# Performance work log

Measured on AMD Instinct MI355X. Metric: run time of the kernel, lower is better.

## Reference

```python
import jax, jax.numpy as jnp
import numpy as np

EMBED_DIM = 1024
KEY_SIZE = 1024
VALUE_SIZE = 1024


def setup_inputs() -> dict:
    key = jax.random.key(0)
    k1, k2, k3, k4, k5 = jax.random.split(key, 5)
    B, L = 4, 4096
    s = 1.0 / np.sqrt(EMBED_DIM)
    return {
        "x": jax.random.normal(k1, (B, L, EMBED_DIM), dtype=jnp.float32),
        # torch nn.Linear weights: [out_features, in_features]
        "Wq": jax.random.normal(k2, (KEY_SIZE, EMBED_DIM), dtype=jnp.float32) * s,
        "Wk": jax.random.normal(k3, (KEY_SIZE, EMBED_DIM), dtype=jnp.float32) * s,
        "Wv": jax.random.normal(k4, (VALUE_SIZE, EMBED_DIM), dtype=jnp.float32) * s,
        "Wo": jax.random.normal(k5, (EMBED_DIM, VALUE_SIZE), dtype=jnp.float32) * s,
    }


def reference(x, Wq, Wk, Wv, Wo):
    # x: [B, L, E]
    q = jnp.einsum("ble,ke->blk", x, Wq)  # [B, L, K]
    k = jnp.einsum("ble,ke->blk", x, Wk)  # [B, L, K]
    v = jnp.einsum("ble,ve->blv", x, Wv)  # [B, L, V]
    K = k.shape[-1]
    # transposed (feature-axial) attention: att over feature dims, contracting seq L
    att = jnp.einsum("blk,blj->bkj", q, k) / jnp.sqrt(jnp.asarray(K, x.dtype))  # [B, K, K]
    att = jax.nn.softmax(att, axis=-1)
    # out[b,l,k] = sum_j att[b,k,j] * v[b,l,j]  (matmul(att, v^T) then transpose)
    out = jnp.einsum("bkj,blj->blk", att, v)  # [B, L, K]
    return jnp.einsum("blv,ev->ble", out, Wo)  # [B, L, E]
```

## Files before the change

### kernel.cpp

```cpp
#include <hip/hip_runtime.h>
#include <hip/hip_bf16.h>

typedef unsigned short u16;
typedef __bf16 bf16x8 __attribute__((ext_vector_type(8)));
typedef float f32x4 __attribute__((ext_vector_type(4)));
typedef unsigned short ushort8 __attribute__((ext_vector_type(8)));

#define AS1 __attribute__((address_space(1)))
#define AS3 __attribute__((address_space(3)))

__device__ inline u16 f2bf(float f) {
  union { float f; unsigned int u; } c; c.f = f;
  unsigned int u = c.u;
  return (u16)((u + 0x7fffu + ((u >> 16) & 1u)) >> 16);
}
__device__ inline float bf2f(u16 v) {
  union { unsigned int u; float f; } c; c.u = ((unsigned int)v) << 16;
  return c.f;
}

__global__ __launch_bounds__(256) void cvt_x_dual(const float* __restrict__ x,
                                                  u16* __restrict__ xbf,
                                                  u16* __restrict__ xT) {
  __shared__ u16 tile[64][68];
  const int t = threadIdx.x;
  const long e0 = (long)blockIdx.x * 64;
  const long l0 = (long)blockIdx.y * 64;
  const long b  = blockIdx.z;
  const int tr = t >> 4, tc = t & 15;
#pragma unroll
  for (int i = 0; i < 4; ++i) {
    const int r = tr + i * 16;
    const long gl = b * 4096 + l0 + r;
    float4 v = *reinterpret_cast<const float4*>(x + gl * 1024 + e0 + tc * 4);
    ushort4 o;
    o.x = f2bf(v.x); o.y = f2bf(v.y); o.z = f2bf(v.z); o.w = f2bf(v.w);
    *reinterpret_cast<ushort4*>(xbf + gl * 1024 + e0 + tc * 4) = o;
    *reinterpret_cast<ushort4*>(&tile[r][tc * 4]) = o;
  }
  __syncthreads();
#pragma unroll
  for (int i = 0; i < 4; ++i) {
    const int c = tr + i * 16;
    ushort4 o;
    o.x = tile[tc * 4 + 0][c]; o.y = tile[tc * 4 + 1][c];
    o.z = tile[tc * 4 + 2][c]; o.w = tile[tc * 4 + 3][c];
    *reinterpret_cast<ushort4*>(xT + b * (1024L * 4096) + (e0 + c) * 4096 + l0 + tc * 4) = o;
  }
}

__global__ __launch_bounds__(256) void cvt_w4(const float* __restrict__ a, const float* __restrict__ b,
                                              const float* __restrict__ c, const float* __restrict__ d,
                                              u16* __restrict__ oa, u16* __restrict__ ob,
                                              u16* __restrict__ oc, u16* __restrict__ od) {
  int i = blockIdx.x * 256 + threadIdx.x;
  const int which = i >> 18;
  const int j = i & 262143;
  const float* src = which == 0 ? a : which == 1 ? b : which == 2 ? c : d;
  u16* dst = which == 0 ? oa : which == 1 ? ob : which == 2 ? oc : od;
  float4 v = reinterpret_cast<const float4*>(src)[j];
  ushort4 o;
  o.x = f2bf(v.x); o.y = f2bf(v.y); o.z = f2bf(v.z); o.w = f2bf(v.w);
  reinterpret_cast<ushort4*>(dst)[j] = o;
}

__global__ __launch_bounds__(256) void transpose_bf16(
    const u16* __restrict__ src, long sLd, long sZ,
    u16* __restrict__ dst, long dLd, long dZ) {
  __shared__ u16 tile[64][68];
  const int t = threadIdx.x;
  const long r0 = (long)blockIdx.y * 64;
  const long c0 = (long)blockIdx.x * 64;
  const long z = blockIdx.z;
  const int tr = t >> 4, tc = t & 15;
#pragma unroll
  for (int i = 0; i < 4; ++i) {
    const int r = tr + i * 16;
    ushort4 v = *reinterpret_cast<const ushort4*>(src + z * sZ + (r0 + r) * sLd + c0 + tc * 4);
    *reinterpret_cast<ushort4*>(&tile[r][tc * 4]) = v;
  }
  __syncthreads();
#pragma unroll
  for (int i = 0; i < 4; ++i) {
    const int c = tr + i * 16;
    ushort4 o;
    o.x = tile[tc * 4 + 0][c]; o.y = tile[tc * 4 + 1][c];
    o.z = tile[tc * 4 + 2][c]; o.w = tile[tc * 4 + 3][c];
    *reinterpret_cast<ushort4*>(dst + z * dZ + (c0 + c) * dLd + r0 + tc * 4) = o;
  }
}

__device__ __forceinline__ void stage_half(const u16* __restrict__ g, long ld, int k0,
                                           u16* dst, int t) {
#pragma unroll
  for (int i = 0; i < 2; ++i) {
    const int c = i * 512 + t;
    const int r = c >> 3;
    const int s = c & 7;
    const int col = ((s ^ (r & 7)) << 3) + k0;
    __builtin_amdgcn_global_load_lds((const AS1 void*)(g + (long)r * ld + col),
                                     (AS3 void*)(dst + c * 8), 16, 0, 0);
  }
}

__device__ __forceinline__ bf16x8 frag_ld(const u16* s, int row, int colb) {
  return *reinterpret_cast<const bf16x8*>(
      reinterpret_cast<const char*>(s) + row * 128 + (colb ^ ((row & 7) << 4)));
}

#define BAR_PRE()       do { asm volatile("s_waitcnt vmcnt(6)" ::: "memory"); \
                             __builtin_amdgcn_s_barrier(); \
                             asm volatile("" ::: "memory"); } while (0)
#define BAR_POST()      do { asm volatile("" ::: "memory"); \
                             __builtin_amdgcn_s_barrier(); \
                             asm volatile("" ::: "memory"); } while (0)

template<bool OUT_F32>
__global__ __launch_bounds__(512, 2) void gemm_nt256(
    const u16* __restrict__ A, long lda, long sAz4, long sAz1,
    const u16* __restrict__ B, long ldb, long sBz4, long sBz1,
    void* __restrict__ Cv, long ldc, long sCz4, long sCz1,
    long cBatch, int cShift,
    int K, float scale)
{
  __shared__ u16 sm[2 * 32768] __attribute__((aligned(16)));

  const int t = threadIdx.x;
  int wg = blockIdx.x + gridDim.x * blockIdx.y;
  const int nwg = gridDim.x * gridDim.y;
  const int qq = nwg >> 3;
  wg = (wg & 7) * qq + (wg >> 3);
  const long m0 = (long)(wg % gridDim.x) * 256;
  const long n0 = (long)(wg / gridDim.x) * 256;
  const int z = blockIdx.z;
  const long azoff = (long)(z >> 2) * sAz4 + (long)(z & 3) * sAz1;
  const long bzoff = (long)(z >> 2) * sBz4 + (long)(z & 3) * sBz1;
  const u16* Ab = A + azoff + m0 * lda;
  const u16* Bb = B + bzoff + n0 * ldb;

  const int wid = t >> 6, lane = t & 63;
  const int lhi = lane >> 4, llo = lane & 15;
  const int wm = wid >> 2, wn = wid & 3;

  f32x4 acc[2][4][2][2] = {};
  const int NT = K >> 6;

  stage_half(Ab, lda, 0, sm, t);
  stage_half(Bb + 128 * ldb, ldb, 0, sm + 16384 + 8192, t);
  stage_half(Bb, ldb, 0, sm + 16384, t);
  stage_half(Ab + 128 * lda, lda, 0, sm + 8192, t);
  stage_half(Ab, lda, 64, sm + 32768, t);
  stage_half(Bb + 128 * ldb, ldb, 64, sm + 32768 + 16384 + 8192, t);
  asm volatile("s_waitcnt vmcnt(4)" ::: "memory");
  __builtin_amdgcn_s_barrier();
  asm volatile("" ::: "memory");

  for (int kt = 0; kt < NT; ++kt) {
    const int kb = kt & 1;
    u16* bc = sm + kb * 32768;
    u16* bn = sm + (kb ^ 1) * 32768;
    const u16* sAc = bc;
    const u16* sBc = bc + 16384;
    const int k1 = ((kt + 1 < NT) ? kt + 1 : 0) << 6;
    const int k2 = ((kt + 2 < NT) ? kt + 2 : kt + 2 - NT) << 6;

    bf16x8 a[4][2], bl[2][2], bh[2][2];

#pragma unroll
    for (int fr = 0; fr < 4; ++fr)
#pragma unroll
      for (int kk = 0; kk < 2; ++kk)
        a[fr][kk] = frag_ld(sAc, wm * 64 + fr * 16 + llo, (kk << 6) + (lhi << 4));
#pragma unroll
    for (int fc = 0; fc < 2; ++fc)
#pragma unroll
      for (int kk = 0; kk < 2; ++kk)
        bl[fc][kk] = frag_ld(sBc, wn * 32 + fc * 16 + llo, (kk << 6) + (lhi << 4));
    stage_half(Bb, ldb, k1, bn + 16384, t);
    BAR_PRE();
    __builtin_amdgcn_s_setprio(1);
#pragma unroll
    for (int fr = 0; fr < 4; ++fr)
#pragma unroll
      for (int fc = 0; fc < 2; ++fc)
#pragma unroll
        for (int kk = 0; kk < 2; ++kk)
          acc[0][fr][0][fc] = __builtin_amdgcn_mfma_f32_16x16x32_bf16(a[fr][kk], bl[fc][kk], acc[0][fr][0][fc], 0, 0, 0);
    __builtin_amdgcn_s_setprio(0);
    BAR_POST();

#pragma unroll
    for (int fc = 0; fc < 2; ++fc)
#pragma unroll
      for (int kk = 0; kk < 2; ++kk)
        bh[fc][kk] = frag_ld(sBc, 128 + wn * 32 + fc * 16 + llo, (kk << 6) + (lhi << 4));
    stage_half(Ab + 128 * lda, lda, k1, bn + 8192, t);
    BAR_PRE();
    __builtin_amdgcn_s_setprio(1);
#pragma unroll
    for (int fr = 0; fr < 4; ++fr)
#pragma unroll
      for (int fc = 0; fc < 2; ++fc)
#pragma unroll
        for (int kk = 0; kk < 2; ++kk)
          acc[0][fr][1][fc] = __builtin_amdgcn_mfma_f32_16x16x32_bf16(a[fr][kk], bh[fc][kk], acc[0][fr][1][fc], 0, 0, 0);
    __builtin_amdgcn_s_setprio(0);
    BAR_POST();

#pragma unroll
    for (int fr = 0; fr < 4; ++fr)
#pragma unroll
      for (int kk = 0; kk < 2; ++kk)
        a[fr][kk] = frag_ld(sAc, 128 + wm * 64 + fr * 16 + llo, (kk << 6) + (lhi << 4));
    stage_half(Ab, lda, k2, bc, t);
    BAR_PRE();
    __builtin_amdgcn_s_setprio(1);
#pragma unroll
    for (int fr = 0; fr < 4; ++fr)
#pragma unroll
      for (int fc = 0; fc < 2; ++fc)
#pragma unroll
        for (int kk = 0; kk < 2; ++kk)
          acc[1][fr][1][fc] = __builtin_amdgcn_mfma_f32_16x16x32_bf16(a[fr][kk], bh[fc][kk], acc[1][fr][1][fc], 0, 0, 0);
    __builtin_amdgcn_s_setprio(0);
    BAR_POST();

    stage_half(Bb + 128 * ldb, ldb, k2, bc + 16384 + 8192, t);
    BAR_PRE();
    __builtin_amdgcn_s_setprio(1);
#pragma unroll
    for (int fr = 0; fr < 4; ++fr)
#pragma unroll
      for (int fc = 0; fc < 2; ++fc)
#pragma unroll
        for (int kk = 0; kk < 2; ++kk)
          acc[1][fr][0][fc] = __builtin_amdgcn_mfma_f32_16x16x32_bf16(a[fr][kk], bl[fc][kk], acc[1][fr][0][fc], 0, 0, 0);
    __builtin_amdgcn_s_setprio(0);
    BAR_POST();
  }

  const long cb = n0 >> cShift;
  const long ncol0 = n0 - (cb << cShift);
  const long czoff = (long)(z >> 2) * sCz4 + (long)(z & 3) * sCz1 + cb * cBatch;
#pragma unroll
  for (int ah = 0; ah < 2; ++ah)
#pragma unroll
    for (int fr = 0; fr < 4; ++fr)
#pragma unroll
      for (int e = 0; e < 4; ++e) {
        const long r = m0 + ah * 128 + wm * 64 + fr * 16 + lhi * 4 + e;
#pragma unroll
        for (int bh2 = 0; bh2 < 2; ++bh2)
#pragma unroll
          for (int fc = 0; fc < 2; ++fc) {
            const long col = ncol0 + bh2 * 128 + wn * 32 + fc * 16 + llo;
            const float val = acc[ah][fr][bh2][fc][e] * scale;
            if (OUT_F32)
              ((float*)Cv)[czoff + r * ldc + col] = val;
            else
              ((u16*)Cv)[czoff + r * ldc + col] = f2bf(val);
          }
      }
}

__device__ __forceinline__ bf16x8 frag_ld128(const u16* s, int row, int lhi) {
  return *reinterpret_cast<const bf16x8*>(
      reinterpret_cast<const char*>(s) + row * 64 + ((lhi ^ (row & 3)) << 4));
}

template<bool OUT_F32>
__global__ __launch_bounds__(512, 2) void gemm_nt128w(
    const u16* __restrict__ A, long lda, long sAz,
    const u16* __restrict__ B, long ldb, long sBz,
    void* __restrict__ Cv, long ldc, long sCz,
    int K, float scale)
{
  __shared__ u16 sm[3 * 8192] __attribute__((aligned(16)));

  const int t = threadIdx.x;
  int wg = blockIdx.x + gridDim.x * blockIdx.y;
  const int nwg = gridDim.x * gridDim.y;
  const int qq = nwg >> 3;
  wg = (wg & 7) * qq + (wg >> 3);
  const long m0 = (long)(wg % gridDim.x) * 128;
  const long n0 = (long)(wg / gridDim.x) * 128;
  const int z = blockIdx.z;
  A += (long)z * sAz + m0 * lda;
  B += (long)z * sBz + n0 * ldb;

  const int wid = t >> 6, lane = t & 63;
  const int lhi = lane >> 4, llo = lane & 15;
  const int wr = (wid >> 2) * 64, wc = (wid & 3) * 32;
  const int srow = t >> 2;
  const int scol = t & 3;

  f32x4 acc[4][2] = {};
  const int NT = K >> 5;

#define STAGEW(kk, buf)                                                                 \
  do {                                                                                  \
    const int col = ((scol ^ (srow & 3)) << 3) + (kk);                                  \
    __builtin_amdgcn_global_load_lds((const AS1 void*)(A + (long)srow * lda + col),     \
                                     (AS3 void*)((buf) + t * 8), 16, 0, 0);             \
    __builtin_amdgcn_global_load_lds((const AS1 void*)(B + (long)srow * ldb + col),     \
                                     (AS3 void*)((buf) + 4096 + t * 8), 16, 0, 0);      \
  } while (0)

  STAGEW(0, sm);
  STAGEW(32, sm + 8192);
  STAGEW(64, sm + 16384);

  for (int kt = 0; kt < NT; ++kt) {
    asm volatile("s_waitcnt vmcnt(4)" ::: "memory");
    __builtin_amdgcn_s_barrier();
    asm volatile("" ::: "memory");
    u16* buf = sm + (kt % 3) * 8192;
    bf16x8 af[4], bfr[2];
#pragma unroll
    for (int i = 0; i < 4; ++i) af[i] = frag_ld128(buf, wr + i * 16 + llo, lhi);
#pragma unroll
    for (int j = 0; j < 2; ++j) bfr[j] = frag_ld128(buf + 4096, wc + j * 16 + llo, lhi);
    __builtin_amdgcn_s_setprio(1);
#pragma unroll
    for (int i = 0; i < 4; ++i)
#pragma unroll
      for (int j = 0; j < 2; ++j)
        acc[i][j] = __builtin_amdgcn_mfma_f32_16x16x32_bf16(af[i], bfr[j], acc[i][j], 0, 0, 0);
    __builtin_amdgcn_s_setprio(0);
    asm volatile("" ::: "memory");
    __builtin_amdgcn_s_barrier();
    asm volatile("" ::: "memory");
    const int k3 = ((kt + 3 < NT) ? kt + 3 : kt + 3 - NT) << 5;
    STAGEW(k3, buf);
  }

#pragma unroll
  for (int i = 0; i < 4; ++i) {
#pragma unroll
    for (int e = 0; e < 4; ++e) {
      const long r = m0 + wr + i * 16 + lhi * 4 + e;
      if (OUT_F32) {
        float* C = (float*)Cv + (long)z * sCz + r * ldc + n0 + wc + llo;
#pragma unroll
        for (int j = 0; j < 2; ++j) C[j * 16] = acc[i][j][e] * scale;
      } else {
        u16* C = (u16*)Cv + (long)z * sCz + r * ldc + n0 + wc + llo;
#pragma unroll
        for (int j = 0; j < 2; ++j) C[j * 16] = f2bf(acc[i][j][e] * scale);
      }
    }
  }
}

__global__ __launch_bounds__(256) void greduce4b(const u16* __restrict__ gp,
                                                 u16* __restrict__ gb) {
  const long o = (long)blockIdx.x * 256 + threadIdx.x;
  const long b = o >> 17;
  const long r = o & 131071;
  float s[8] = {};
#pragma unroll
  for (int p = 0; p < 4; ++p) {
    ushort8 u = reinterpret_cast<const ushort8*>(gp)[((b * 4 + p) << 17) + r];
#pragma unroll
    for (int j = 0; j < 8; ++j) s[j] += bf2f(u[j]);
  }
  ushort8 out;
#pragma unroll
  for (int j = 0; j < 8; ++j) out[j] = f2bf(s[j]);
  reinterpret_cast<ushort8*>(gb)[o] = out;
}

__global__ __launch_bounds__(256) void softmax1(const float* __restrict__ att,
                                                u16* __restrict__ P) {
  const long row = blockIdx.x;
  const int t = threadIdx.x;
  float4 v = reinterpret_cast<const float4*>(att + row * 1024)[t];
  float m = fmaxf(fmaxf(v.x, v.y), fmaxf(v.z, v.w));
#pragma unroll
  for (int off = 32; off > 0; off >>= 1) m = fmaxf(m, __shfl_down(m, off, 64));
  __shared__ float smax[4], ssum[4];
  const int wid = t >> 6, lane = t & 63;
  if (lane == 0) smax[wid] = m;
  __syncthreads();
  m = fmaxf(fmaxf(smax[0], smax[1]), fmaxf(smax[2], smax[3]));
  float e0 = expf(v.x - m), e1 = expf(v.y - m), e2 = expf(v.z - m), e3 = expf(v.w - m);
  float s = e0 + e1 + e2 + e3;
#pragma unroll
  for (int off = 32; off > 0; off >>= 1) s += __shfl_down(s, off, 64);
  if (lane == 0) ssum[wid] = s;
  __syncthreads();
  s = ssum[0] + ssum[1] + ssum[2] + ssum[3];
  float inv = 1.0f / s;
  ushort4 o;
  o.x = f2bf(e0 * inv); o.y = f2bf(e1 * inv); o.z = f2bf(e2 * inv); o.w = f2bf(e3 * inv);
  reinterpret_cast<ushort4*>(P + row * 1024)[t] = o;
}

extern "C" void kernel_launch(void* const* d_in, const int* in_sizes, int n_in,
                              void* d_out, int out_size, void* d_ws, size_t ws_size,
                              hipStream_t stream) {
  const float* x  = (const float*)d_in[0];
  const float* Wq = (const float*)d_in[1];
  const float* Wk = (const float*)d_in[2];
  const float* Wv = (const float*)d_in[3];
  const float* Wo = (const float*)d_in[4];

  const long M1 = 1L << 20;

  u16* xbf    = (u16*)d_ws;
  u16* wq     = xbf + 16 * M1;
  u16* wk     = wq + M1;
  u16* wv     = wk + M1;
  u16* wo     = wv + M1;
  u16* wvT    = wo + M1;
  u16* xT     = wvT + M1;
  u16* gbf    = xT + 16 * M1;
  u16* tbuf   = gbf + 4 * M1;
  u16* pbuf   = tbuf + 4 * M1;
  u16* rtb    = pbuf + 4 * M1;
  u16* sbuf   = rtb + 4 * M1;
  u16* gpartb = sbuf + 4 * M1;
  float* attf = (float*)d_out;

  dim3 b256(256), b512(512);
  const long NOF = 0;
  const int NSH = 30;

  cvt_x_dual<<<dim3(16, 64, 4), b256, 0, stream>>>(x, xbf, xT);
  cvt_w4<<<dim3(4096), b256, 0, stream>>>(Wq, Wk, Wv, Wo, wq, wk, wv, wo);
  transpose_bf16<<<dim3(16, 16, 1), b256, 0, stream>>>(wv, 1024, 0, wvT, 1024, 0);

  gemm_nt256<false><<<dim3(4, 4, 16), b512, 0, stream>>>(
      xT, 4096, 1024L * 4096, 1024, xT, 4096, 1024L * 4096, 1024,
      (void*)gpartb, 1024, 4L << 20, 1L << 20, NOF, NSH, 1024, 1.0f);
  greduce4b<<<dim3(2048), b256, 0, stream>>>(gpartb, gbf);

  gemm_nt128w<false><<<dim3(8, 8, 4), b512, 0, stream>>>(
      wq, 1024, 0, gbf, 1024, M1, (void*)tbuf, 1024, M1, 1024, 1.0f);
  gemm_nt128w<true><<<dim3(8, 8, 4), b512, 0, stream>>>(
      tbuf, 1024, M1, wk, 1024, 0, (void*)attf, 1024, M1, 1024, 1.0f / 32.0f);
  softmax1<<<dim3(4096), b256, 0, stream>>>(attf, pbuf);

  gemm_nt128w<false><<<dim3(8, 8, 4), b512, 0, stream>>>(
      wvT, 1024, 0, pbuf, 1024, M1, (void*)rtb, 1024, M1, 1024, 1.0f);
  gemm_nt128w<false><<<dim3(8, 8, 4), b512, 0, stream>>>(
      wo, 1024, 0, rtb, 1024, M1, (void*)sbuf, 1024, M1, 1024, 1.0f);

  gemm_nt256<true><<<dim3(16, 4, 4), b512, 0, stream>>>(
      xbf, 1024, 0, 4096L * 1024, sbuf, 1024, 0, M1,
      d_out, 1024, 0, 4096L * 1024, NOF, NSH, 1024, 1.0f);
}
```

Before: 197.3 us.

## Widen 128-tile GEMM K-step to 64 and swizzle XCD mapping across batch

The 128x128 GEMM kernel now stages 64-wide K slices per buffer instead of 32, reusing the 128-byte swizzled staging and fragment loads from the 256 kernel. This halves the number of barrier-separated iterations and doubles MFMA work per sync, at the cost of triple-buffered LDS growing to 96KB, which may limit occupancy to one block per CU. Both GEMM kernels also fold blockIdx.z into the XCD round-robin remap so batch slices spread across chiplets.

```diff
diff --git a/kernel.cpp b/kernel.cpp
--- a/kernel.cpp
+++ b/kernel.cpp
@@ -108,6 +108,17 @@
       reinterpret_cast<const char*>(s) + row * 128 + (colb ^ ((row & 7) << 4)));
 }
 
+#define XCD_DECODE(TILE)                                                     \
+  const int nxy = gridDim.x * gridDim.y;                                     \
+  int flat = blockIdx.x + gridDim.x * blockIdx.y + nxy * blockIdx.z;         \
+  const int total = nxy * gridDim.z;                                         \
+  const int qq = total >> 3;                                                 \
+  flat = (flat & 7) * qq + (flat >> 3);                                      \
+  const int z = flat / nxy;                                                  \
+  const int wg = flat % nxy;                                                 \
+  const long m0 = (long)(wg % gridDim.x) * (TILE);                           \
+  const long n0 = (long)(wg / gridDim.x) * (TILE);
+
 #define BAR_PRE()       do { asm volatile("s_waitcnt vmcnt(6)" ::: "memory"); \
                              __builtin_amdgcn_s_barrier(); \
                              asm volatile("" ::: "memory"); } while (0)
@@ -126,13 +137,7 @@
   __shared__ u16 sm[2 * 32768] __attribute__((aligned(16)));
 
   const int t = threadIdx.x;
-  int wg = blockIdx.x + gridDim.x * blockIdx.y;
-  const int nwg = gridDim.x * gridDim.y;
-  const int qq = nwg >> 3;
-  wg = (wg & 7) * qq + (wg >> 3);
-  const long m0 = (long)(wg % gridDim.x) * 256;
-  const long n0 = (long)(wg / gridDim.x) * 256;
-  const int z = blockIdx.z;
+  XCD_DECODE(256);
   const long azoff = (long)(z >> 2) * sAz4 + (long)(z & 3) * sAz1;
   const long bzoff = (long)(z >> 2) * sBz4 + (long)(z & 3) * sBz1;
   const u16* Ab = A + azoff + m0 * lda;
@@ -263,11 +268,6 @@
       }
 }
 
-__device__ __forceinline__ bf16x8 frag_ld128(const u16* s, int row, int lhi) {
-  return *reinterpret_cast<const bf16x8*>(
-      reinterpret_cast<const char*>(s) + row * 64 + ((lhi ^ (row & 3)) << 4));
-}
-
 template<bool OUT_F32>
 __global__ __launch_bounds__(512, 2) void gemm_nt128w(
     const u16* __restrict__ A, long lda, long sAz,
@@ -275,63 +275,58 @@
     void* __restrict__ Cv, long ldc, long sCz,
     int K, float scale)
 {
-  __shared__ u16 sm[3 * 8192] __attribute__((aligned(16)));
+  __shared__ u16 sm[3 * 16384] __attribute__((aligned(16)));
 
   const int t = threadIdx.x;
-  int wg = blockIdx.x + gridDim.x * blockIdx.y;
-  const int nwg = gridDim.x * gridDim.y;
-  const int qq = nwg >> 3;
-  wg = (wg & 7) * qq + (wg >> 3);
-  const long m0 = (long)(wg % gridDim.x) * 128;
-  const long n0 = (long)(wg / gridDim.x) * 128;
-  const int z = blockIdx.z;
+  XCD_DECODE(128);
   A += (long)z * sAz + m0 * lda;
   B += (long)z * sBz + n0 * ldb;
 
   const int wid = t >> 6, lane = t & 63;
   const int lhi = lane >> 4, llo = lane & 15;
   const int wr = (wid >> 2) * 64, wc = (wid & 3) * 32;
-  const int srow = t >> 2;
-  const int scol = t & 3;
 
   f32x4 acc[4][2] = {};
-  const int NT = K >> 5;
-
-#define STAGEW(kk, buf)                                                                 \
-  do {                                                                                  \
-    const int col = ((scol ^ (srow & 3)) << 3) + (kk);                                  \
-    __builtin_amdgcn_global_load_lds((const AS1 void*)(A + (long)srow * lda + col),     \
-                                     (AS3 void*)((buf) + t * 8), 16, 0, 0);             \
-    __builtin_amdgcn_global_load_lds((const AS1 void*)(B + (long)srow * ldb + col),     \
-                                     (AS3 void*)((buf) + 4096 + t * 8), 16, 0, 0);      \
-  } while (0)
-
-  STAGEW(0, sm);
-  STAGEW(32, sm + 8192);
-  STAGEW(64, sm + 16384);
+  const int NT = K >> 6;
+
+  stage_half(A, lda, 0, sm, t);
+  stage_half(B, ldb, 0, sm + 8192, t);
+  stage_half(A, lda, 64, sm + 16384, t);
+  stage_half(B, ldb, 64, sm + 16384 + 8192, t);
+  stage_half(A, lda, 128, sm + 32768, t);
+  stage_half(B, ldb, 128, sm + 32768 + 8192, t);
 
   for (int kt = 0; kt < NT; ++kt) {
-    asm volatile("s_waitcnt vmcnt(4)" ::: "memory");
+    asm volatile("s_waitcnt vmcnt(8)" ::: "memory");
     __builtin_amdgcn_s_barrier();
     asm volatile("" ::: "memory");
-    u16* buf = sm + (kt % 3) * 8192;
-    bf16x8 af[4], bfr[2];
-#pragma unroll
-    for (int i = 0; i < 4; ++i) af[i] = frag_ld128(buf, wr + i * 16 + llo, lhi);
-#pragma unroll
-    for (int j = 0; j < 2; ++j) bfr[j] = frag_ld128(buf + 4096, wc + j * 16 + llo, lhi);
+    u16* buf = sm + (kt % 3) * 16384;
+    bf16x8 af[4][2], bfr[2][2];
+#pragma unroll
+    for (int i = 0; i < 4; ++i)
+#pragma unroll
+      for (int kk = 0; kk < 2; ++kk)
+        af[i][kk] = frag_ld(buf, wr + i * 16 + llo, (kk << 6) + (lhi << 4));
+#pragma unroll
+    for (int j = 0; j < 2; ++j)
+#pragma unroll
+      for (int kk = 0; kk < 2; ++kk)
+        bfr[j][kk] = frag_ld(buf + 8192, wc + j * 16 + llo, (kk << 6) + (lhi << 4));
     __builtin_amdgcn_s_setprio(1);
 #pragma unroll
     for (int i = 0; i < 4; ++i)
 #pragma unroll
       for (int j = 0; j < 2; ++j)
-        acc[i][j] = __builtin_amdgcn_mfma_f32_16x16x32_bf16(af[i], bfr[j], acc[i][j], 0, 0, 0);
+#pragma unroll
+        for (int kk = 0; kk < 2; ++kk)
+          acc[i][j] = __builtin_amdgcn_mfma_f32_16x16x32_bf16(af[i][kk], bfr[j][kk], acc[i][j], 0, 0, 0);
     __builtin_amdgcn_s_setprio(0);
     asm volatile("" ::: "memory");
     __builtin_amdgcn_s_barrier();
     asm volatile("" ::: "memory");
-    const int k3 = ((kt + 3 < NT) ? kt + 3 : kt + 3 - NT) << 5;
-    STAGEW(k3, buf);
+    const int k3 = ((kt + 3 < NT) ? kt + 3 : kt + 3 - NT) << 6;
+    stage_half(A, lda, k3, buf, t);
+    stage_half(B, ldb, k3, buf + 8192, t);
   }
 
 #pragma unroll
```

Result: faster. 190.2 us (-3.6%).
